# Kernel optimization log

Hardware: AMD Instinct MI355X
Metric: run time of the kernel (lower is better)

## Reference

```python
import jax, jax.numpy as jnp
import numpy as np

D_MODEL = 1024
H = 16
D_K = D_MODEL // H
WINDOW = 256
NEG = -1e9


def setup_inputs() -> dict:
    key = jax.random.key(0)
    ks = jax.random.split(key, 7)
    B, S = 2, 4096
    sc = 0.02
    return {
        "q": jax.random.normal(ks[0], (B, S, D_MODEL), jnp.float32),
        "k": jax.random.normal(ks[1], (B, S, D_MODEL), jnp.float32),
        "v": jax.random.normal(ks[2], (B, S, D_MODEL), jnp.float32),
        "wq": jax.random.normal(ks[3], (D_MODEL, D_MODEL), jnp.float32) * sc,
        "wk": jax.random.normal(ks[4], (D_MODEL, D_MODEL), jnp.float32) * sc,
        "wv": jax.random.normal(ks[5], (D_MODEL, D_MODEL), jnp.float32) * sc,
        "wo": jax.random.normal(ks[6], (D_MODEL, D_MODEL), jnp.float32) * sc,
    }


def _local_mask(seq_len: int, window_size: int):
    left = (window_size - 1) // 2
    right = window_size - 1 - left
    idx = jnp.arange(seq_len)
    dist = jnp.abs(idx[None, :] - idx[:, None])
    return (dist <= left) | (dist <= right)  # [S, S] bool


def reference(q, k, v, wq, wk, wv, wo):
    B, S, _ = q.shape
    # torch Linear: x @ W.T
    def proj(x, w):
        return (x @ w.T).reshape(B, S, H, D_K).transpose(0, 2, 1, 3)  # [B,H,S,Dk]
    Q, K, V = proj(q, wq), proj(k, wk), proj(v, wv)
    scores = jnp.einsum("bhqd,bhkd->bhqk", Q, K) / jnp.sqrt(jnp.float32(D_K))
    mask = _local_mask(S, WINDOW)
    scores = jnp.where(mask[None, None], scores, NEG)
    attn = jax.nn.softmax(scores, axis=-1)
    x = jnp.einsum("bhqk,bhkd->bhqd", attn, V)
    x = x.transpose(0, 2, 1, 3).reshape(B, S, D_MODEL)
    return x @ wo.T
```

## Files before the change

### kernel.cpp

```cpp
#include <hip/hip_runtime.h>
#include <hip/hip_bf16.h>

#define S_LEN 4096
#define B_SZ 2
#define DM 1024
#define NH 16
#define DH 64

typedef __attribute__((ext_vector_type(8))) short short8;
typedef __attribute__((ext_vector_type(4))) float f32x4;

__device__ __forceinline__ ushort f2b(float f) {
  union { __hip_bfloat16 b; ushort u; } cv;
  cv.b = __float2bfloat16(f);
  return cv.u;
}

__device__ __forceinline__ void glds16(const ushort* g, ushort* l) {
  __builtin_amdgcn_global_load_lds(
      (const __attribute__((address_space(1))) void*)g,
      (__attribute__((address_space(3))) void*)l, 16, 0, 0);
}

__global__ void cvt_all(const float* __restrict__ q, const float* __restrict__ k,
                        const float* __restrict__ v, const float* __restrict__ wq,
                        const float* __restrict__ wk, const float* __restrict__ wv,
                        const float* __restrict__ wo, ushort* __restrict__ dst) {
  const int NX4 = 2097152;
  const int NW4 = 262144;
  const int total = 3 * NX4 + 4 * NW4;
  for (int i = blockIdx.x * blockDim.x + threadIdx.x; i < total;
       i += gridDim.x * blockDim.x) {
    const float* s;
    int j;
    if (i < NX4) { s = q; j = i; }
    else if (i < 2 * NX4) { s = k; j = i - NX4; }
    else if (i < 3 * NX4) { s = v; j = i - 2 * NX4; }
    else {
      int t = i - 3 * NX4;
      int wsel = t >> 18;
      j = t & (NW4 - 1);
      s = wsel == 0 ? wq : wsel == 1 ? wk : wsel == 2 ? wv : wo;
    }
    float4 val = reinterpret_cast<const float4*>(s)[j];
    ushort4 o;
    o.x = f2b(val.x); o.y = f2b(val.y); o.z = f2b(val.z); o.w = f2b(val.w);
    reinterpret_cast<ushort4*>(dst)[i] = o;
  }
}

__device__ __forceinline__ short8 ldsrd(const ushort* base, int row, int cb) {
  const int pcb = cb ^ ((row & 7) << 4);
  return *reinterpret_cast<const short8*>(
      reinterpret_cast<const char*>(base) + row * 128 + pcb);
}

template <int MODE>
__launch_bounds__(512, 2)
__global__ void gemmP(const ushort* __restrict__ A0, const ushort* __restrict__ A1,
                      const ushort* __restrict__ A2, const ushort* __restrict__ W0,
                      const ushort* __restrict__ W1, const ushort* __restrict__ W2,
                      void* __restrict__ O0, void* __restrict__ O1,
                      void* __restrict__ O2) {
  __shared__ ushort As[3][16384];
  __shared__ ushort Bs[3][8192];
  const int tid = threadIdx.x;
  const int lane = tid & 63, w = tid >> 6;
  const int wm = w >> 1, wn = w & 1;
  const int g = lane >> 4, lr = lane & 15;
  const int m0 = blockIdx.x * 256;
  const int ysel = (MODE == 0) ? (blockIdx.y >> 3) : 0;
  const ushort* A = (MODE == 0) ? (ysel == 0 ? A0 : ysel == 1 ? A1 : A2) : A0;
  const ushort* W = (MODE == 0) ? (ysel == 0 ? W0 : ysel == 1 ? W1 : W2) : W0;
  const int n0 = ((MODE == 0) ? (blockIdx.y & 7) : blockIdx.y) * 128;

  const int row_r = tid >> 3;
  const int cb = ((tid & 7) * 16) ^ ((row_r & 7) << 4);
  const ushort* Asrc = A + (size_t)(m0 + row_r) * DM + (cb >> 1);
  const ushort* Wsrc = W + (size_t)(n0 + row_r) * DM + (cb >> 1);

#define STG_ALL(bs, kt)                                                      \
  { const int kq = (kt) * 64;                                                \
    glds16(Asrc + kq,                        &As[bs][w * 512]);              \
    glds16(Asrc + (size_t)64 * DM + kq,      &As[bs][4096 + w * 512]);       \
    glds16(Asrc + (size_t)128 * DM + kq,     &As[bs][8192 + w * 512]);       \
    glds16(Asrc + (size_t)192 * DM + kq,     &As[bs][12288 + w * 512]);      \
    glds16(Wsrc + kq,                        &Bs[bs][w * 512]);              \
    glds16(Wsrc + (size_t)64 * DM + kq,      &Bs[bs][4096 + w * 512]); }

  f32x4 acc[4][4] = {};
  short8 af[4][2], b0[2][2], b1[2][2];

  STG_ALL(0, 0);
  STG_ALL(1, 1);

  int bc = 0;
  for (int kt = 0; kt < 16; ++kt) {
    const int bs = bc >= 1 ? bc - 1 : bc + 2;
    const int tn = kt + 2 < 16 ? kt + 2 : 15;
    asm volatile("s_waitcnt vmcnt(6)" ::: "memory");
    __builtin_amdgcn_s_barrier();
    __builtin_amdgcn_sched_barrier(0);
    const ushort* Ab = &As[bc][0];
    const ushort* Bb = &Bs[bc][0];
#pragma unroll
    for (int m = 0; m < 4; m++)
#pragma unroll
      for (int kk = 0; kk < 2; kk++)
        af[m][kk] = ldsrd(Ab, wm * 64 + m * 16 + lr, kk * 64 + g * 16);
#pragma unroll
    for (int n = 0; n < 2; n++)
#pragma unroll
      for (int kk = 0; kk < 2; kk++) {
        b0[n][kk] = ldsrd(Bb, wn * 64 + n * 16 + lr, kk * 64 + g * 16);
        b1[n][kk] = ldsrd(Bb, wn * 64 + 32 + n * 16 + lr, kk * 64 + g * 16);
      }
    STG_ALL(bs, tn);
    __builtin_amdgcn_sched_barrier(0);
    asm volatile("s_waitcnt lgkmcnt(0)" ::: "memory");
    __builtin_amdgcn_sched_barrier(0);
    __builtin_amdgcn_s_setprio(1);
#pragma unroll
    for (int m = 0; m < 4; m++)
#pragma unroll
      for (int n = 0; n < 2; n++)
#pragma unroll
        for (int kk = 0; kk < 2; kk++)
          acc[m][n] = __builtin_amdgcn_mfma_f32_16x16x32_bf16(af[m][kk], b0[n][kk],
                                                              acc[m][n], 0, 0, 0);
#pragma unroll
    for (int m = 0; m < 4; m++)
#pragma unroll
      for (int n = 0; n < 2; n++)
#pragma unroll
        for (int kk = 0; kk < 2; kk++)
          acc[m][2 + n] = __builtin_amdgcn_mfma_f32_16x16x32_bf16(af[m][kk], b1[n][kk],
                                                                  acc[m][2 + n], 0, 0, 0);
    __builtin_amdgcn_s_setprio(0);
    __builtin_amdgcn_sched_barrier(0);
    bc = bc + 1 == 3 ? 0 : bc + 1;
  }
#undef STG_ALL

  const int colB = n0 + wn * 64;
#pragma unroll
  for (int m = 0; m < 4; ++m) {
    const int row0 = m0 + wm * 64 + m * 16 + g * 4;
#pragma unroll
    for (int n = 0; n < 4; ++n) {
      const int col = colB + n * 16 + lr;
      if (MODE == 2) {
#pragma unroll
        for (int r = 0; r < 4; r++)
          reinterpret_cast<float*>(O0)[(size_t)(row0 + r) * DM + col] = acc[m][n][r];
      } else if (ysel == 0 || ysel == 1) {
        ushort* O = reinterpret_cast<ushort*>(ysel == 0 ? O0 : O1);
#pragma unroll
        for (int r = 0; r < 4; r++)
          O[(size_t)(row0 + r) * DM + col] = f2b(acc[m][n][r]);
      } else {
        const int b = row0 >> 12, s0 = row0 & 4095;
        const int h = col >> 6, dk = col & 63;
        ushort4 o;
        o.x = f2b(acc[m][n][0]); o.y = f2b(acc[m][n][1]);
        o.z = f2b(acc[m][n][2]); o.w = f2b(acc[m][n][3]);
        *reinterpret_cast<ushort4*>(
            reinterpret_cast<ushort*>(O2) +
            (((size_t)(b * NH + h) * DH + dk) << 12) + s0) = o;
      }
    }
  }
}

__global__ void attn_local(const ushort* __restrict__ Qp, const ushort* __restrict__ Kp,
                           const ushort* __restrict__ Vt, ushort* __restrict__ Ao) {
  __shared__ ushort Ks[2][4096];
  __shared__ ushort Vs[2][4096];
  __shared__ ushort Ps[4][16 * 72];
  const int tid = threadIdx.x;
  const int lane = tid & 63;
  const int w = tid >> 6;
  const int g = lane >> 4, lr = lane & 15;
  const int bh = blockIdx.y, b = bh >> 4, h = bh & 15;
  const int q0 = blockIdx.x * 64;

  const int qrow = q0 + w * 16 + lr;
  const ushort* qptr = Qp + ((size_t)b * S_LEN + qrow) * DM + h * DH;
  short8 qf[2];
  qf[0] = *reinterpret_cast<const short8*>(qptr + g * 8);
  qf[1] = *reinterpret_cast<const short8*>(qptr + 32 + g * 8);

  float m_r[4], l_r[4];
  f32x4 acc_o[4] = {};
#pragma unroll
  for (int r = 0; r < 4; r++) { m_r[r] = -1e30f; l_r[r] = 0.f; }

  const int sr = tid >> 3;
  const int scb = (tid & 7) * 16;

  const int t_lo = q0 >= 128 ? q0 - 128 : 0;
  const int t_hi = (q0 + 192) <= S_LEN ? (q0 + 192) : S_LEN;

#define STAGE(bb, kk0)                                                        \
  {                                                                           \
    _Pragma("unroll")                                                         \
    for (int i = 0; i < 2; i++) {                                             \
      const int row = i * 32 + sr;                                            \
      const int cbk = scb ^ ((row & 7) << 4);                                 \
      glds16(Kp + ((size_t)b * S_LEN + (kk0) + row) * DM + h * DH + cbk / 2,  \
             &Ks[bb][i * 2048 + w * 512]);                                    \
      glds16(Vt + (((size_t)bh * DH + row) << 12) + (kk0) + cbk / 2,          \
             &Vs[bb][i * 2048 + w * 512]);                                    \
    }                                                                         \
  }

  STAGE(0, t_lo);

  int it = 0;
  for (int k0 = t_lo; k0 < t_hi; k0 += 64, ++it) {
    const int cur = it & 1;
    const bool pf = (k0 + 64 < t_hi);
    if (pf) {
      STAGE(cur ^ 1, k0 + 64);
      asm volatile("s_waitcnt vmcnt(4)" ::: "memory");
    } else {
      asm volatile("s_waitcnt vmcnt(0)" ::: "memory");
    }
    __builtin_amdgcn_sched_barrier(0);
    __builtin_amdgcn_s_barrier();
    __builtin_amdgcn_sched_barrier(0);

    f32x4 sc[4] = {};
#pragma unroll
    for (int kk = 0; kk < 2; kk++) {
#pragma unroll
      for (int nt = 0; nt < 4; nt++) {
        const int kr = nt * 16 + lr;
        const int cbk = (kk * 64 + g * 16) ^ ((kr & 7) << 4);
        short8 kf = *reinterpret_cast<const short8*>(
            reinterpret_cast<const char*>(&Ks[cur][0]) + kr * 128 + cbk);
        sc[nt] = __builtin_amdgcn_mfma_f32_16x16x32_bf16(qf[kk], kf, sc[nt], 0, 0, 0);
      }
    }
    const bool edge = (k0 < q0 - 64) || (k0 > q0 + 64);
    float mx[4] = {-1e30f, -1e30f, -1e30f, -1e30f};
    if (edge) {
#pragma unroll
      for (int nt = 0; nt < 4; nt++) {
        const int key = k0 + nt * 16 + lr;
#pragma unroll
        for (int r = 0; r < 4; r++) {
          const int qr = q0 + w * 16 + g * 4 + r;
          int d = qr - key; d = d < 0 ? -d : d;
          float s = (d <= 128) ? sc[nt][r] * 0.125f : -1e9f;
          sc[nt][r] = s;
          mx[r] = fmaxf(mx[r], s);
        }
      }
    } else {
#pragma unroll
      for (int nt = 0; nt < 4; nt++)
#pragma unroll
        for (int r = 0; r < 4; r++) {
          const float s = sc[nt][r] * 0.125f;
          sc[nt][r] = s;
          mx[r] = fmaxf(mx[r], s);
        }
    }
#pragma unroll
    for (int r = 0; r < 4; r++) {
      mx[r] = fmaxf(mx[r], __shfl_xor(mx[r], 1));
      mx[r] = fmaxf(mx[r], __shfl_xor(mx[r], 2));
      mx[r] = fmaxf(mx[r], __shfl_xor(mx[r], 4));
      mx[r] = fmaxf(mx[r], __shfl_xor(mx[r], 8));
    }
    float fac[4], rs[4];
#pragma unroll
    for (int r = 0; r < 4; r++) {
      const float mn = fmaxf(m_r[r], mx[r]);
      fac[r] = __expf(m_r[r] - mn);
      m_r[r] = mn;
      rs[r] = 0.f;
    }
#pragma unroll
    for (int nt = 0; nt < 4; nt++)
#pragma unroll
      for (int r = 0; r < 4; r++) {
        const float p = __expf(sc[nt][r] - m_r[r]);
        sc[nt][r] = p;
        rs[r] += p;
      }
#pragma unroll
    for (int r = 0; r < 4; r++) {
      rs[r] += __shfl_xor(rs[r], 1);
      rs[r] += __shfl_xor(rs[r], 2);
      rs[r] += __shfl_xor(rs[r], 4);
      rs[r] += __shfl_xor(rs[r], 8);
      l_r[r] = l_r[r] * fac[r] + rs[r];
    }
#pragma unroll
    for (int nt = 0; nt < 4; nt++)
#pragma unroll
      for (int r = 0; r < 4; r++)
        acc_o[nt][r] *= fac[r];

    ushort* myP = Ps[w];
#pragma unroll
    for (int nt = 0; nt < 4; nt++)
#pragma unroll
      for (int r = 0; r < 4; r++)
        myP[(g * 4 + r) * 72 + nt * 16 + lr] = f2b(sc[nt][r]);
    asm volatile("s_waitcnt lgkmcnt(0)" ::: "memory");
    __builtin_amdgcn_sched_barrier(0);

#pragma unroll
    for (int kk = 0; kk < 2; kk++) {
      short8 pf2 = *reinterpret_cast<const short8*>(myP + lr * 72 + kk * 32 + g * 8);
#pragma unroll
      for (int nt = 0; nt < 4; nt++) {
        const int vr = nt * 16 + lr;
        const int cbk = (kk * 64 + g * 16) ^ ((vr & 7) << 4);
        short8 vf = *reinterpret_cast<const short8*>(
            reinterpret_cast<const char*>(&Vs[cur][0]) + vr * 128 + cbk);
        acc_o[nt] = __builtin_amdgcn_mfma_f32_16x16x32_bf16(pf2, vf, acc_o[nt], 0, 0, 0);
      }
    }
    __builtin_amdgcn_sched_barrier(0);
    __builtin_amdgcn_s_barrier();
    __builtin_amdgcn_sched_barrier(0);
  }
#undef STAGE

  const int qr0 = q0 + w * 16 + g * 4;
  ushort* orow = Ao + (size_t)b * S_LEN * DM + h * DH;
#pragma unroll
  for (int nt = 0; nt < 4; nt++)
#pragma unroll
    for (int r = 0; r < 4; r++)
      orow[(size_t)(qr0 + r) * DM + nt * 16 + lr] = f2b(acc_o[nt][r] / l_r[r]);
}

extern "C" void kernel_launch(void* const* d_in, const int* in_sizes, int n_in,
                              void* d_out, int out_size, void* d_ws, size_t ws_size,
                              hipStream_t stream) {
  const float* q  = (const float*)d_in[0];
  const float* k  = (const float*)d_in[1];
  const float* v  = (const float*)d_in[2];
  const float* wq = (const float*)d_in[3];
  const float* wk = (const float*)d_in[4];
  const float* wv = (const float*)d_in[5];
  const float* wo = (const float*)d_in[6];

  const size_t NX = (size_t)B_SZ * S_LEN * DM;
  const size_t NW = (size_t)DM * DM;
  if (ws_size < (7 * NX + 4 * NW) * sizeof(ushort)) return;

  ushort* ws  = (ushort*)d_ws;
  ushort* qb  = ws;
  ushort* kb  = qb + NX;
  ushort* vb  = kb + NX;
  ushort* wqb = vb + NX;
  ushort* wkb = wqb + NW;
  ushort* wvb = wkb + NW;
  ushort* wob = wvb + NW;
  ushort* Qp  = wob + NW;
  ushort* Kp  = Qp + NX;
  ushort* Vt  = Kp + NX;
  ushort* Ao  = Vt + NX;

  cvt_all<<<dim3(2048), dim3(256), 0, stream>>>(q, k, v, wq, wk, wv, wo, ws);

  gemmP<0><<<dim3(32, 24), dim3(512), 0, stream>>>(qb, kb, vb, wqb, wkb, wvb,
                                                   Qp, Kp, Vt);

  attn_local<<<dim3(64, 32), dim3(256), 0, stream>>>(Qp, Kp, Vt, Ao);

  gemmP<2><<<dim3(32, 8), dim3(512), 0, stream>>>(Ao, Ao, Ao, wob, wob, wob,
                                                  d_out, d_out, d_out);
}
```

Before: 160.3 us.

## Fuse fp32-to-bf16 activation conversion into QKV GEMM A-tile loading

The separate pass that converted q/k/v to bf16 is removed. The QKV projection GEMM now loads fp32 A tiles into registers, packs them to bf16 and writes them into swizzled LDS itself, with register prefetch one tile ahead and a double-buffered A tile. Only the weights still go through a conversion kernel. This avoids writing and re-reading about 48 MB of bf16 activation copies, but launch bounds drop to one block per CU and each A-tile stage now costs VGPRs plus VALU conversion work. The attention loop is also reordered to wait, barrier, then prefetch, so it needs one barrier per iteration instead of two.

Result: faster. 154.4 us (-3.7%).

```diff
diff --git a/kernel.cpp b/kernel.cpp
--- a/kernel.cpp
+++ b/kernel.cpp
@@ -16,93 +16,111 @@
   return cv.u;
 }
 
+__device__ __forceinline__ short8 pack8(float4 a, float4 b) {
+  short8 r;
+  r[0] = (short)f2b(a.x); r[1] = (short)f2b(a.y);
+  r[2] = (short)f2b(a.z); r[3] = (short)f2b(a.w);
+  r[4] = (short)f2b(b.x); r[5] = (short)f2b(b.y);
+  r[6] = (short)f2b(b.z); r[7] = (short)f2b(b.w);
+  return r;
+}
+
 __device__ __forceinline__ void glds16(const ushort* g, ushort* l) {
   __builtin_amdgcn_global_load_lds(
       (const __attribute__((address_space(1))) void*)g,
       (__attribute__((address_space(3))) void*)l, 16, 0, 0);
 }
 
-__global__ void cvt_all(const float* __restrict__ q, const float* __restrict__ k,
-                        const float* __restrict__ v, const float* __restrict__ wq,
-                        const float* __restrict__ wk, const float* __restrict__ wv,
-                        const float* __restrict__ wo, ushort* __restrict__ dst) {
-  const int NX4 = 2097152;
-  const int NW4 = 262144;
-  const int total = 3 * NX4 + 4 * NW4;
-  for (int i = blockIdx.x * blockDim.x + threadIdx.x; i < total;
-       i += gridDim.x * blockDim.x) {
-    const float* s;
-    int j;
-    if (i < NX4) { s = q; j = i; }
-    else if (i < 2 * NX4) { s = k; j = i - NX4; }
-    else if (i < 3 * NX4) { s = v; j = i - 2 * NX4; }
-    else {
-      int t = i - 3 * NX4;
-      int wsel = t >> 18;
-      j = t & (NW4 - 1);
-      s = wsel == 0 ? wq : wsel == 1 ? wk : wsel == 2 ? wv : wo;
-    }
-    float4 val = reinterpret_cast<const float4*>(s)[j];
-    ushort4 o;
-    o.x = f2b(val.x); o.y = f2b(val.y); o.z = f2b(val.z); o.w = f2b(val.w);
-    reinterpret_cast<ushort4*>(dst)[i] = o;
-  }
-}
-
 __device__ __forceinline__ short8 ldsrd(const ushort* base, int row, int cb) {
   const int pcb = cb ^ ((row & 7) << 4);
   return *reinterpret_cast<const short8*>(
       reinterpret_cast<const char*>(base) + row * 128 + pcb);
 }
-
-template <int MODE>
-__launch_bounds__(512, 2)
-__global__ void gemmP(const ushort* __restrict__ A0, const ushort* __restrict__ A1,
-                      const ushort* __restrict__ A2, const ushort* __restrict__ W0,
-                      const ushort* __restrict__ W1, const ushort* __restrict__ W2,
-                      void* __restrict__ O0, void* __restrict__ O1,
-                      void* __restrict__ O2) {
-  __shared__ ushort As[3][16384];
-  __shared__ ushort Bs[3][8192];
+__device__ __forceinline__ void ldswr(ushort* base, int row, int cb, short8 v) {
+  const int pcb = cb ^ ((row & 7) << 4);
+  *reinterpret_cast<short8*>(reinterpret_cast<char*>(base) + row * 128 + pcb) = v;
+}
+
+__global__ void cvt_w(const float* __restrict__ wq, const float* __restrict__ wk,
+                      const float* __restrict__ wv, const float* __restrict__ wo,
+                      ushort* __restrict__ dst) {
+  const int NW4 = 262144;
+  for (int i = blockIdx.x * blockDim.x + threadIdx.x; i < 4 * NW4;
+       i += gridDim.x * blockDim.x) {
+    const int wsel = i >> 18;
+    const int j = i & (NW4 - 1);
+    const float* s = wsel == 0 ? wq : wsel == 1 ? wk : wsel == 2 ? wv : wo;
+    float4 v = reinterpret_cast<const float4*>(s)[j];
+    ushort4 o;
+    o.x = f2b(v.x); o.y = f2b(v.y); o.z = f2b(v.z); o.w = f2b(v.w);
+    reinterpret_cast<ushort4*>(dst)[i] = o;
+  }
+}
+
+__launch_bounds__(512, 1)
+__global__ void gemmQKV(const float* __restrict__ Af0, const float* __restrict__ Af1,
+                        const float* __restrict__ Af2, const ushort* __restrict__ Wall,
+                        ushort* __restrict__ O0, ushort* __restrict__ O1,
+                        ushort* __restrict__ O2) {
+  __shared__ ushort As[2][16384];
+  __shared__ ushort Ws[3][8192];
   const int tid = threadIdx.x;
   const int lane = tid & 63, w = tid >> 6;
   const int wm = w >> 1, wn = w & 1;
   const int g = lane >> 4, lr = lane & 15;
   const int m0 = blockIdx.x * 256;
-  const int ysel = (MODE == 0) ? (blockIdx.y >> 3) : 0;
-  const ushort* A = (MODE == 0) ? (ysel == 0 ? A0 : ysel == 1 ? A1 : A2) : A0;
-  const ushort* W = (MODE == 0) ? (ysel == 0 ? W0 : ysel == 1 ? W1 : W2) : W0;
-  const int n0 = ((MODE == 0) ? (blockIdx.y & 7) : blockIdx.y) * 128;
-
-  const int row_r = tid >> 3;
-  const int cb = ((tid & 7) * 16) ^ ((row_r & 7) << 4);
-  const ushort* Asrc = A + (size_t)(m0 + row_r) * DM + (cb >> 1);
-  const ushort* Wsrc = W + (size_t)(n0 + row_r) * DM + (cb >> 1);
-
-#define STG_ALL(bs, kt)                                                      \
-  { const int kq = (kt) * 64;                                                \
-    glds16(Asrc + kq,                        &As[bs][w * 512]);              \
-    glds16(Asrc + (size_t)64 * DM + kq,      &As[bs][4096 + w * 512]);       \
-    glds16(Asrc + (size_t)128 * DM + kq,     &As[bs][8192 + w * 512]);       \
-    glds16(Asrc + (size_t)192 * DM + kq,     &As[bs][12288 + w * 512]);      \
-    glds16(Wsrc + kq,                        &Bs[bs][w * 512]);              \
-    glds16(Wsrc + (size_t)64 * DM + kq,      &Bs[bs][4096 + w * 512]); }
+  const int ysel = blockIdx.y >> 3;
+  const float* A = ysel == 0 ? Af0 : ysel == 1 ? Af1 : Af2;
+  const ushort* W = Wall + (size_t)ysel * (DM * DM);
+  const int n0 = (blockIdx.y & 7) * 128;
+
+  const int c8 = tid & 7, rb = tid >> 3;
+  const float* Ab0 = A + (size_t)(m0 + rb) * DM + c8 * 8;
+  const int wcb = ((tid & 7) * 16) ^ ((rb & 7) << 4);
+  const ushort* Wsrc = W + (size_t)(n0 + rb) * DM + (wcb >> 1);
+
+  float4 ar[8];
+
+#define LDA(t)                                                                \
+  { const int kq = (t) * 64;                                                  \
+    _Pragma("unroll")                                                         \
+    for (int j = 0; j < 4; j++) {                                             \
+      const float* p = Ab0 + (size_t)(64 * j) * DM + kq;                      \
+      ar[2 * j] = *reinterpret_cast<const float4*>(p);                        \
+      ar[2 * j + 1] = *reinterpret_cast<const float4*>(p + 4);                \
+    } }
+#define DSWA(b)                                                               \
+  { _Pragma("unroll")                                                         \
+    for (int j = 0; j < 4; j++)                                               \
+      ldswr(As[b], rb + 64 * j, c8 * 16, pack8(ar[2 * j], ar[2 * j + 1])); }
+#define STGW(wb, t)                                                           \
+  { const int kq = (t) * 64;                                                  \
+    glds16(Wsrc + kq, &Ws[wb][w * 512]);                                      \
+    glds16(Wsrc + (size_t)64 * DM + kq, &Ws[wb][4096 + w * 512]); }
 
   f32x4 acc[4][4] = {};
   short8 af[4][2], b0[2][2], b1[2][2];
 
-  STG_ALL(0, 0);
-  STG_ALL(1, 1);
-
-  int bc = 0;
+  LDA(0);
+  STGW(0, 0);
+  STGW(1, 1);
+  DSWA(0);
+  LDA(1);
+  asm volatile("s_waitcnt lgkmcnt(0)" ::: "memory");
+  __builtin_amdgcn_sched_barrier(0);
+  __builtin_amdgcn_s_barrier();
+  __builtin_amdgcn_sched_barrier(0);
+
+  int wb = 0;
   for (int kt = 0; kt < 16; ++kt) {
-    const int bs = bc >= 1 ? bc - 1 : bc + 2;
+    const int cur = kt & 1;
+    const int wbn = wb >= 1 ? wb - 1 : wb + 2;
     const int tn = kt + 2 < 16 ? kt + 2 : 15;
-    asm volatile("s_waitcnt vmcnt(6)" ::: "memory");
+    asm volatile("s_waitcnt vmcnt(10)" ::: "memory");
     __builtin_amdgcn_s_barrier();
     __builtin_amdgcn_sched_barrier(0);
-    const ushort* Ab = &As[bc][0];
-    const ushort* Bb = &Bs[bc][0];
+    const ushort* Ab = &As[cur][0];
+    const ushort* Bb = &Ws[wb][0];
 #pragma unroll
     for (int m = 0; m < 4; m++)
 #pragma unroll
@@ -115,7 +133,9 @@
         b0[n][kk] = ldsrd(Bb, wn * 64 + n * 16 + lr, kk * 64 + g * 16);
         b1[n][kk] = ldsrd(Bb, wn * 64 + 32 + n * 16 + lr, kk * 64 + g * 16);
       }
-    STG_ALL(bs, tn);
+    DSWA(cur ^ 1);
+    LDA(tn);
+    STGW(wbn, tn);
     __builtin_amdgcn_sched_barrier(0);
     asm volatile("s_waitcnt lgkmcnt(0)" ::: "memory");
     __builtin_amdgcn_sched_barrier(0);
@@ -138,9 +158,11 @@
                                                                   acc[m][2 + n], 0, 0, 0);
     __builtin_amdgcn_s_setprio(0);
     __builtin_amdgcn_sched_barrier(0);
-    bc = bc + 1 == 3 ? 0 : bc + 1;
-  }
-#undef STG_ALL
+    wb = wb + 1 == 3 ? 0 : wb + 1;
+  }
+#undef LDA
+#undef DSWA
+#undef STGW
 
   const int colB = n0 + wn * 64;
 #pragma unroll
@@ -149,12 +171,8 @@
 #pragma unroll
     for (int n = 0; n < 4; ++n) {
       const int col = colB + n * 16 + lr;
-      if (MODE == 2) {
-#pragma unroll
-        for (int r = 0; r < 4; r++)
-          reinterpret_cast<float*>(O0)[(size_t)(row0 + r) * DM + col] = acc[m][n][r];
-      } else if (ysel == 0 || ysel == 1) {
-        ushort* O = reinterpret_cast<ushort*>(ysel == 0 ? O0 : O1);
+      if (ysel == 0 || ysel == 1) {
+        ushort* O = ysel == 0 ? O0 : O1;
 #pragma unroll
         for (int r = 0; r < 4; r++)
           O[(size_t)(row0 + r) * DM + col] = f2b(acc[m][n][r]);
@@ -165,9 +183,102 @@
         o.x = f2b(acc[m][n][0]); o.y = f2b(acc[m][n][1]);
         o.z = f2b(acc[m][n][2]); o.w = f2b(acc[m][n][3]);
         *reinterpret_cast<ushort4*>(
-            reinterpret_cast<ushort*>(O2) +
-            (((size_t)(b * NH + h) * DH + dk) << 12) + s0) = o;
-      }
+            O2 + (((size_t)(b * NH + h) * DH + dk) << 12) + s0) = o;
+      }
+    }
+  }
+}
+
+__launch_bounds__(512, 2)
+__global__ void gemmOut(const ushort* __restrict__ A, const ushort* __restrict__ W,
+                        float* __restrict__ Of) {
+  __shared__ ushort As[3][16384];
+  __shared__ ushort Bs[3][8192];
+  const int tid = threadIdx.x;
+  const int lane = tid & 63, w = tid >> 6;
+  const int wm = w >> 1, wn = w & 1;
+  const int g = lane >> 4, lr = lane & 15;
+  const int m0 = blockIdx.x * 256;
+  const int n0 = blockIdx.y * 128;
+
+  const int row_r = tid >> 3;
+  const int cb = ((tid & 7) * 16) ^ ((row_r & 7) << 4);
+  const ushort* Asrc = A + (size_t)(m0 + row_r) * DM + (cb >> 1);
+  const ushort* Wsrc = W + (size_t)(n0 + row_r) * DM + (cb >> 1);
+
+#define STG_ALL(bs, kt)                                                      \
+  { const int kq = (kt) * 64;                                                \
+    glds16(Asrc + kq,                        &As[bs][w * 512]);              \
+    glds16(Asrc + (size_t)64 * DM + kq,      &As[bs][4096 + w * 512]);       \
+    glds16(Asrc + (size_t)128 * DM + kq,     &As[bs][8192 + w * 512]);       \
+    glds16(Asrc + (size_t)192 * DM + kq,     &As[bs][12288 + w * 512]);      \
+    glds16(Wsrc + kq,                        &Bs[bs][w * 512]);              \
+    glds16(Wsrc + (size_t)64 * DM + kq,      &Bs[bs][4096 + w * 512]); }
+
+  f32x4 acc[4][4] = {};
+  short8 af[4][2], b0[2][2], b1[2][2];
+
+  STG_ALL(0, 0);
+  STG_ALL(1, 1);
+
+  int bc = 0;
+  for (int kt = 0; kt < 16; ++kt) {
+    const int bs = bc >= 1 ? bc - 1 : bc + 2;
+    const int tn = kt + 2 < 16 ? kt + 2 : 15;
+    asm volatile("s_waitcnt vmcnt(6)" ::: "memory");
+    __builtin_amdgcn_s_barrier();
+    __builtin_amdgcn_sched_barrier(0);
+    const ushort* Ab = &As[bc][0];
+    const ushort* Bb = &Bs[bc][0];
+#pragma unroll
+    for (int m = 0; m < 4; m++)
+#pragma unroll
+      for (int kk = 0; kk < 2; kk++)
+        af[m][kk] = ldsrd(Ab, wm * 64 + m * 16 + lr, kk * 64 + g * 16);
+#pragma unroll
+    for (int n = 0; n < 2; n++)
+#pragma unroll
+      for (int kk = 0; kk < 2; kk++) {
+        b0[n][kk] = ldsrd(Bb, wn * 64 + n * 16 + lr, kk * 64 + g * 16);
+        b1[n][kk] = ldsrd(Bb, wn * 64 + 32 + n * 16 + lr, kk * 64 + g * 16);
+      }
+    STG_ALL(bs, tn);
+    __builtin_amdgcn_sched_barrier(0);
+    asm volatile("s_waitcnt lgkmcnt(0)" ::: "memory");
+    __builtin_amdgcn_sched_barrier(0);
+    __builtin_amdgcn_s_setprio(1);
+#pragma unroll
+    for (int m = 0; m < 4; m++)
+#pragma unroll
+      for (int n = 0; n < 2; n++)
+#pragma unroll
+        for (int kk = 0; kk < 2; kk++)
+          acc[m][n] = __builtin_amdgcn_mfma_f32_16x16x32_bf16(af[m][kk], b0[n][kk],
+                                                              acc[m][n], 0, 0, 0);
+#pragma unroll
+    for (int m = 0; m < 4; m++)
+#pragma unroll
+      for (int n = 0; n < 2; n++)
+#pragma unroll
+        for (int kk = 0; kk < 2; kk++)
+          acc[m][2 + n] = __builtin_amdgcn_mfma_f32_16x16x32_bf16(af[m][kk], b1[n][kk],
+                                                                  acc[m][2 + n], 0, 0, 0);
+    __builtin_amdgcn_s_setprio(0);
+    __builtin_amdgcn_sched_barrier(0);
+    bc = bc + 1 == 3 ? 0 : bc + 1;
+  }
+#undef STG_ALL
+
+  const int colB = n0 + wn * 64;
+#pragma unroll
+  for (int m = 0; m < 4; ++m) {
+    const int row0 = m0 + wm * 64 + m * 16 + g * 4;
+#pragma unroll
+    for (int n = 0; n < 4; ++n) {
+      const int col = colB + n * 16 + lr;
+#pragma unroll
+      for (int r = 0; r < 4; r++)
+        Of[(size_t)(row0 + r) * DM + col] = acc[m][n][r];
     }
   }
 }
@@ -219,15 +330,10 @@
   int it = 0;
   for (int k0 = t_lo; k0 < t_hi; k0 += 64, ++it) {
     const int cur = it & 1;
-    const bool pf = (k0 + 64 < t_hi);
-    if (pf) {
-      STAGE(cur ^ 1, k0 + 64);
-      asm volatile("s_waitcnt vmcnt(4)" ::: "memory");
-    } else {
-      asm volatile("s_waitcnt vmcnt(0)" ::: "memory");
-    }
-    __builtin_amdgcn_sched_barrier(0);
+    asm volatile("s_waitcnt vmcnt(0)" ::: "memory");
     __builtin_amdgcn_s_barrier();
+    __builtin_amdgcn_sched_barrier(0);
+    if (k0 + 64 < t_hi) STAGE(cur ^ 1, k0 + 64);
     __builtin_amdgcn_sched_barrier(0);
 
     f32x4 sc[4] = {};
@@ -325,9 +431,6 @@
         acc_o[nt] = __builtin_amdgcn_mfma_f32_16x16x32_bf16(pf2, vf, acc_o[nt], 0, 0, 0);
       }
     }
-    __builtin_amdgcn_sched_barrier(0);
-    __builtin_amdgcn_s_barrier();
-    __builtin_amdgcn_sched_barrier(0);
   }
 #undef STAGE
 
@@ -353,28 +456,21 @@
 
   const size_t NX = (size_t)B_SZ * S_LEN * DM;
   const size_t NW = (size_t)DM * DM;
-  if (ws_size < (7 * NX + 4 * NW) * sizeof(ushort)) return;
+  if (ws_size < (4 * NX + 4 * NW) * sizeof(ushort)) return;
 
   ushort* ws  = (ushort*)d_ws;
-  ushort* qb  = ws;
-  ushort* kb  = qb + NX;
-  ushort* vb  = kb + NX;
-  ushort* wqb = vb + NX;
-  ushort* wkb = wqb + NW;
-  ushort* wvb = wkb + NW;
-  ushort* wob = wvb + NW;
-  ushort* Qp  = wob + NW;
+  ushort* wqb = ws;
+  ushort* wob = wqb + 3 * NW;
+  ushort* Qp  = wqb + 4 * NW;
   ushort* Kp  = Qp + NX;
   ushort* Vt  = Kp + NX;
   ushort* Ao  = Vt + NX;
 
-  cvt_all<<<dim3(2048), dim3(256), 0, stream>>>(q, k, v, wq, wk, wv, wo, ws);
-
-  gemmP<0><<<dim3(32, 24), dim3(512), 0, stream>>>(qb, kb, vb, wqb, wkb, wvb,
-                                                   Qp, Kp, Vt);
+  cvt_w<<<dim3(2048), dim3(256), 0, stream>>>(wq, wk, wv, wo, wqb);
+
+  gemmQKV<<<dim3(32, 24), dim3(512), 0, stream>>>(q, k, v, wqb, Qp, Kp, Vt);
 
   attn_local<<<dim3(64, 32), dim3(256), 0, stream>>>(Qp, Kp, Vt, Ao);
 
-  gemmP<2><<<dim3(32, 8), dim3(512), 0, stream>>>(Ao, Ao, Ao, wob, wob, wob,
-                                                  d_out, d_out, d_out);
-}
+  gemmOut<<<dim3(32, 8), dim3(512), 0, stream>>>(Ao, wob, (float*)d_out);
+}
```
